# Performance work log

Hardware: AMD Instinct MI355X
Metric: run time of the kernel (lower is better)

The kernel has to match this reference:

```python
import jax, jax.numpy as jnp
import numpy as np

BATCH = 64
N_FEAT = 50000
UNITS = 1024
NNZ = 2_000_000


def setup_inputs() -> dict:
    key = jax.random.key(0)
    k1, k2, k3, k4 = jax.random.split(key, 4)
    x = jax.random.normal(k1, (BATCH, N_FEAT), dtype=jnp.float32)
    # one trainable weight per nonzero of the sparse kernel
    w = jax.random.normal(k2, (NNZ,), dtype=jnp.float32) * 0.02
    row_idx = jax.random.randint(k3, (NNZ,), 0, N_FEAT, dtype=jnp.int32)
    col_idx = jax.random.randint(k4, (NNZ,), 0, UNITS, dtype=jnp.int32)
    return {"x": x, "w": w, "row_idx": row_idx, "col_idx": col_idx}


def reference(x, w, row_idx, col_idx):
    # out[b, u] = sum_{k : col_idx[k]==u} x[b, row_idx[k]] * w[k]
    # == tf.sparse.sparse_dense_matmul(x, SparseTensor(indices, w, [N_FEAT, UNITS]))
    vals = x[:, row_idx] * w  # [batch, nnz] gather + elementwise scale
    out = jnp.zeros((x.shape[0], UNITS), dtype=x.dtype).at[:, col_idx].add(vals)
    return out
```

## Files before the change

### kernel.cpp

```cpp
#include <hip/hip_runtime.h>
#include <hip/hip_bf16.h>

#define BATCH 64
#define UNITS 1024
#define CHUNK 8192
#define JB 32

typedef unsigned int u32;
typedef unsigned short u16;

__global__ __launch_bounds__(256)
void zero4_kernel(uint4* __restrict__ p, int n4) {
    int i = blockIdx.x * 256 + threadIdx.x;
    const int stride = gridDim.x * 256;
    const uint4 z = make_uint4(0u, 0u, 0u, 0u);
    for (; i < n4; i += stride) p[i] = z;
}

__global__ __launch_bounds__(256)
void prep_kernel(const float* __restrict__ x, u16* __restrict__ xT,
                 const int* __restrict__ col, u32* __restrict__ hist2,
                 int nfeat, int nT, int nnz) {
    __shared__ float tile[64][65];
    __shared__ u32 lh[UNITS];
    const int bid = blockIdx.x;
    const int tid = threadIdx.x;
    if (bid < nT) {
        const int c0 = bid * 64;
        const int tx = tid & 63, ty = tid >> 6;
        for (int b = ty; b < 64; b += 4) {
            int c = c0 + tx;
            if (c < nfeat) tile[b][tx] = x[(size_t)b * nfeat + c];
        }
        __syncthreads();
        for (int i = ty; i < 64; i += 4) {
            int c = c0 + i;
            if (c < nfeat) {
                __hip_bfloat16 h = __float2bfloat16(tile[tx][i]);
                xT[(size_t)c * 64 + tx] = *(u16*)&h;
            }
        }
    } else {
        const int g = bid - nT;
        for (int i = tid; i < UNITS; i += 256) lh[i] = 0u;
        __syncthreads();
        const int g0 = g * CHUNK;
        const int n = min(CHUNK, nnz - g0);
        for (int i = tid; i < n; i += 256)
            atomicAdd(&lh[col[g0 + i]], 1u);
        __syncthreads();
        for (int c = tid; c < UNITS; c += 256)
            hist2[(size_t)g * UNITS + c] = lh[c];
    }
}

__global__ __launch_bounds__(1024)
void scanA_kernel(const u32* __restrict__ hist2, u32* __restrict__ partial,
                  int nchunk) {
    const int j = blockIdx.x, c = threadIdx.x;
    const int gs = j * JB, ge = min(gs + JB, nchunk);
    u32 s = 0;
#pragma unroll 8
    for (int g = gs; g < ge; ++g) s += hist2[(size_t)g * UNITS + c];
    partial[(size_t)j * UNITS + c] = s;
}

__global__ __launch_bounds__(1024)
void scanB_kernel(const u32* __restrict__ partial, u32* __restrict__ jb,
                  u32* __restrict__ col_start, int nblk) {
    const int c = threadIdx.x;
    u32 tot = 0;
    for (int j = 0; j < nblk; ++j) tot += partial[(size_t)j * UNITS + c];
    __shared__ u32 a[UNITS];
    a[c] = tot;
    __syncthreads();
    for (int off = 1; off < UNITS; off <<= 1) {
        u32 add = (c >= off) ? a[c - off] : 0u;
        u32 v = a[c];
        __syncthreads();
        a[c] = v + add;
        __syncthreads();
    }
    u32 run = a[c] - tot;
    col_start[c] = run;
    if (c == UNITS - 1) col_start[UNITS] = a[UNITS - 1];
    for (int j = 0; j < nblk; ++j) {
        jb[(size_t)j * UNITS + c] = run;
        run += partial[(size_t)j * UNITS + c];
    }
}

__global__ __launch_bounds__(512)
void reorder_kernel(const int* __restrict__ row, const int* __restrict__ col,
                    const float* __restrict__ w, const u32* __restrict__ hist2,
                    const u32* __restrict__ jb, u32* __restrict__ sorted, int nnz) {
    __shared__ u32 cur[UNITS];
    const int tid = threadIdx.x;
    const int g = blockIdx.x;
    const int j = g / JB, gs = j * JB;
    for (int c = tid; c < UNITS; c += 512) {
        u32 v = jb[(size_t)j * UNITS + c];
#pragma unroll 4
        for (int gp = gs; gp < g; ++gp) v += hist2[(size_t)gp * UNITS + c];
        cur[c] = v;
    }
    __syncthreads();
    const int g0 = g * CHUNK;
    const int n = min(CHUNK, nnz - g0);
#pragma unroll 4
    for (int i = tid; i < n; i += 512) {
        const int k = g0 + i;
        const u32 c = (u32)col[k];
        __hip_bfloat16 h = __float2bfloat16(w[k]);
        const u32 pk = ((u32)(*(const u16*)&h) << 16) | (u32)row[k];
        const u32 lo = atomicAdd(&cur[c], 1u);
        sorted[lo] = pk;
    }
}

__global__ __launch_bounds__(256)
void gather_kernel(const u16* __restrict__ xTu, const u32* __restrict__ sorted,
                   const u32* __restrict__ col_start, float* __restrict__ out) {
    const int u = blockIdx.x;
    const int tid = threadIdx.x;
    const int wv = tid >> 6, lane = tid & 63;
    const u32 s = col_start[u], e = col_start[u + 1];
    float acc0 = 0.f, acc1 = 0.f, acc2 = 0.f, acc3 = 0.f;
    for (u32 b0 = s + (u32)wv * 64u; b0 < e; b0 += 256u) {
        u32 pk = 0u;
        if (b0 + (u32)lane < e) pk = sorted[b0 + (u32)lane];
#pragma unroll
        for (int t = 0; t < 64; t += 4) {
            const u32 e0 = (u32)__builtin_amdgcn_readlane((int)pk, t);
            const u32 e1 = (u32)__builtin_amdgcn_readlane((int)pk, t + 1);
            const u32 e2 = (u32)__builtin_amdgcn_readlane((int)pk, t + 2);
            const u32 e3 = (u32)__builtin_amdgcn_readlane((int)pk, t + 3);
            const float x0 = __uint_as_float(((u32)xTu[(size_t)(e0 & 0xffffu) * 64 + lane]) << 16);
            const float x1 = __uint_as_float(((u32)xTu[(size_t)(e1 & 0xffffu) * 64 + lane]) << 16);
            const float x2 = __uint_as_float(((u32)xTu[(size_t)(e2 & 0xffffu) * 64 + lane]) << 16);
            const float x3 = __uint_as_float(((u32)xTu[(size_t)(e3 & 0xffffu) * 64 + lane]) << 16);
            acc0 = fmaf(x0, __uint_as_float(e0 & 0xffff0000u), acc0);
            acc1 = fmaf(x1, __uint_as_float(e1 & 0xffff0000u), acc1);
            acc2 = fmaf(x2, __uint_as_float(e2 & 0xffff0000u), acc2);
            acc3 = fmaf(x3, __uint_as_float(e3 & 0xffff0000u), acc3);
        }
    }
    float tot = (acc0 + acc1) + (acc2 + acc3);
    __shared__ float red[4][64];
    red[wv][lane] = tot;
    __syncthreads();
    if (wv == 0)
        out[(size_t)lane * UNITS + u] =
            red[0][lane] + red[1][lane] + red[2][lane] + red[3][lane];
}

__global__ __launch_bounds__(1024, 1)
void scatter_fallback_kernel(const u16* __restrict__ xT, const float* __restrict__ w,
                             const int* __restrict__ row_idx, const int* __restrict__ col_idx,
                             float* __restrict__ out, int nnz) {
    extern __shared__ float priv[];
    const int tid = threadIdx.x;
    for (int i = tid; i < 32 * UNITS; i += 1024) priv[i] = 0.0f;
    __syncthreads();
    const int bid = blockIdx.x, half = bid >> 7, wgIdx = bid & 127;
    const int wave = tid >> 6, lane = tid & 63, h = lane >> 5, bl = lane & 31;
    const int per = (nnz + 127) >> 7;
    const int k0 = wgIdx * per, kend = min(k0 + per, nnz);
    const u16* xTh = xT + half * 32 + bl;
    for (int k = k0 + wave * 2 + h; k < kend; k += 32) {
        const int r = row_idx[k], c = col_idx[k];
        const float xv = __uint_as_float(((u32)xTh[(size_t)r * 64]) << 16);
        atomicAdd(&priv[c * 32 + bl], xv * w[k]);
    }
    __syncthreads();
    for (int i = tid; i < 32 * UNITS; i += 1024) {
        int c = i >> 5, b = half * 32 + (i & 31);
        unsafeAtomicAdd(&out[b * UNITS + c], priv[i]);
    }
}

__global__ __launch_bounds__(256)
void fallback_kernel(const float* __restrict__ x, const float* __restrict__ w,
                     const int* __restrict__ row_idx, const int* __restrict__ col_idx,
                     float* __restrict__ out, int nnz, int nfeat) {
    const int nwaves = (gridDim.x * blockDim.x) >> 6;
    const int wid = (blockIdx.x * blockDim.x + threadIdx.x) >> 6;
    const int lane = threadIdx.x & 63;
    for (int k = wid; k < nnz; k += nwaves) {
        const int r = row_idx[k], c = col_idx[k];
        unsafeAtomicAdd(&out[lane * UNITS + c], x[(size_t)lane * nfeat + r] * w[k]);
    }
}

static inline size_t align256(size_t v) { return (v + 255) & ~(size_t)255; }

extern "C" void kernel_launch(void* const* d_in, const int* in_sizes, int n_in,
                              void* d_out, int out_size, void* d_ws, size_t ws_size,
                              hipStream_t stream) {
    const float* x       = (const float*)d_in[0];
    const float* w       = (const float*)d_in[1];
    const int*   row_idx = (const int*)d_in[2];
    const int*   col_idx = (const int*)d_in[3];
    float*       out     = (float*)d_out;
    const int    nnz     = in_sizes[1];
    const int    nfeat   = in_sizes[0] / BATCH;
    const int    nchunk  = (nnz + CHUNK - 1) / CHUNK;
    const int    nblk    = (nchunk + JB - 1) / JB;
    const int    nT      = (nfeat + 63) / 64;

    const size_t xT_bytes = (size_t)nfeat * 64 * sizeof(u16);
    size_t o = align256(xT_bytes);
    const size_t sorted_off = o;  o = align256(o + (size_t)nnz * sizeof(u32));
    const size_t hist2_off  = o;  o = align256(o + (size_t)nchunk * UNITS * sizeof(u32));
    const size_t part_off   = o;  o = align256(o + (size_t)nblk * UNITS * sizeof(u32));
    const size_t jb_off     = o;  o = align256(o + (size_t)nblk * UNITS * sizeof(u32));
    const size_t cs_off     = o;  o = align256(o + (UNITS + 1) * sizeof(u32));

    if (ws_size >= o && nfeat <= 65536 && nblk <= 64) {
        u16* xT        = (u16*)d_ws;
        u32* sorted    = (u32*)((char*)d_ws + sorted_off);
        u32* hist2     = (u32*)((char*)d_ws + hist2_off);
        u32* partial   = (u32*)((char*)d_ws + part_off);
        u32* jb        = (u32*)((char*)d_ws + jb_off);
        u32* col_start = (u32*)((char*)d_ws + cs_off);

        prep_kernel<<<nT + nchunk, 256, 0, stream>>>(x, xT, col_idx, hist2,
                                                     nfeat, nT, nnz);
        scanA_kernel<<<nblk, 1024, 0, stream>>>(hist2, partial, nchunk);
        scanB_kernel<<<1, 1024, 0, stream>>>(partial, jb, col_start, nblk);
        reorder_kernel<<<nchunk, 512, 0, stream>>>(row_idx, col_idx, w, hist2,
                                                   jb, sorted, nnz);
        gather_kernel<<<UNITS, 256, 0, stream>>>(xT, sorted, col_start, out);
    } else if (ws_size >= xT_bytes) {
        u16* xT = (u16*)d_ws;
        const int nOut4 = (out_size * 4 + 15) / 16;
        zero4_kernel<<<64, 256, 0, stream>>>((uint4*)out, nOut4);
        dim3 tb(256);
        prep_kernel<<<nT, 256, 0, stream>>>(x, xT, col_idx, nullptr, nfeat, nT, 0);
        scatter_fallback_kernel<<<256, 1024, 32 * UNITS * sizeof(float), stream>>>(
            xT, w, row_idx, col_idx, out, nnz);
    } else {
        const int nOut4 = (out_size * 4 + 15) / 16;
        zero4_kernel<<<64, 256, 0, stream>>>((uint4*)out, nOut4);
        fallback_kernel<<<2048, 256, 0, stream>>>(x, w, row_idx, col_idx, out, nnz, nfeat);
    }
}
```

Before: 140.1 us.

## Split gather per unit across four blocks with atomic reduction; batch reorder loads

The gather kernel now launches four blocks per output unit. Each block takes an interleaved quarter of that unit's sorted nonzeros, and the results are combined with float atomic adds into an output that is zeroed beforehand. This raises parallelism from 1024 blocks to 4096, which helps fill the GPU. In exchange it adds a zeroing kernel launch and global atomics, and the summation order becomes nondeterministic. Separately, the reorder kernel's full-chunk path batches eight loads before issuing its LDS atomics and stores, to increase memory-level parallelism.

```diff
diff --git a/kernel.cpp b/kernel.cpp
--- a/kernel.cpp
+++ b/kernel.cpp
@@ -5,6 +5,7 @@
 #define UNITS 1024
 #define CHUNK 8192
 #define JB 32
+#define NSPLIT 4
 
 typedef unsigned int u32;
 typedef unsigned short u16;
@@ -107,26 +108,43 @@
     __syncthreads();
     const int g0 = g * CHUNK;
     const int n = min(CHUNK, nnz - g0);
-#pragma unroll 4
-    for (int i = tid; i < n; i += 512) {
-        const int k = g0 + i;
-        const u32 c = (u32)col[k];
-        __hip_bfloat16 h = __float2bfloat16(w[k]);
-        const u32 pk = ((u32)(*(const u16*)&h) << 16) | (u32)row[k];
-        const u32 lo = atomicAdd(&cur[c], 1u);
-        sorted[lo] = pk;
+    if (n == CHUNK) {
+        for (int j2 = 0; j2 < CHUNK / 512; j2 += 8) {
+            u32 cc[8], pk[8], lo[8];
+#pragma unroll
+            for (int q = 0; q < 8; ++q) {
+                const int k = g0 + tid + 512 * (j2 + q);
+                cc[q] = (u32)col[k];
+                __hip_bfloat16 h = __float2bfloat16(w[k]);
+                pk[q] = ((u32)(*(const u16*)&h) << 16) | (u32)row[k];
+            }
+#pragma unroll
+            for (int q = 0; q < 8; ++q) lo[q] = atomicAdd(&cur[cc[q]], 1u);
+#pragma unroll
+            for (int q = 0; q < 8; ++q) sorted[lo[q]] = pk[q];
+        }
+    } else {
+        for (int i = tid; i < n; i += 512) {
+            const int k = g0 + i;
+            const u32 c = (u32)col[k];
+            __hip_bfloat16 h = __float2bfloat16(w[k]);
+            const u32 pk = ((u32)(*(const u16*)&h) << 16) | (u32)row[k];
+            const u32 lo = atomicAdd(&cur[c], 1u);
+            sorted[lo] = pk;
+        }
     }
 }
 
 __global__ __launch_bounds__(256)
 void gather_kernel(const u16* __restrict__ xTu, const u32* __restrict__ sorted,
                    const u32* __restrict__ col_start, float* __restrict__ out) {
-    const int u = blockIdx.x;
+    const int u = blockIdx.x >> 2;
+    const int part = blockIdx.x & 3;
     const int tid = threadIdx.x;
     const int wv = tid >> 6, lane = tid & 63;
     const u32 s = col_start[u], e = col_start[u + 1];
     float acc0 = 0.f, acc1 = 0.f, acc2 = 0.f, acc3 = 0.f;
-    for (u32 b0 = s + (u32)wv * 64u; b0 < e; b0 += 256u) {
+    for (u32 b0 = s + (u32)(part * 4 + wv) * 64u; b0 < e; b0 += (u32)(NSPLIT * 4) * 64u) {
         u32 pk = 0u;
         if (b0 + (u32)lane < e) pk = sorted[b0 + (u32)lane];
 #pragma unroll
@@ -135,10 +153,14 @@
             const u32 e1 = (u32)__builtin_amdgcn_readlane((int)pk, t + 1);
             const u32 e2 = (u32)__builtin_amdgcn_readlane((int)pk, t + 2);
             const u32 e3 = (u32)__builtin_amdgcn_readlane((int)pk, t + 3);
-            const float x0 = __uint_as_float(((u32)xTu[(size_t)(e0 & 0xffffu) * 64 + lane]) << 16);
-            const float x1 = __uint_as_float(((u32)xTu[(size_t)(e1 & 0xffffu) * 64 + lane]) << 16);
-            const float x2 = __uint_as_float(((u32)xTu[(size_t)(e2 & 0xffffu) * 64 + lane]) << 16);
-            const float x3 = __uint_as_float(((u32)xTu[(size_t)(e3 & 0xffffu) * 64 + lane]) << 16);
+            const u16* p0 = xTu + ((e0 & 0xffffu) << 6);
+            const u16* p1 = xTu + ((e1 & 0xffffu) << 6);
+            const u16* p2 = xTu + ((e2 & 0xffffu) << 6);
+            const u16* p3 = xTu + ((e3 & 0xffffu) << 6);
+            const float x0 = __uint_as_float(((u32)p0[lane]) << 16);
+            const float x1 = __uint_as_float(((u32)p1[lane]) << 16);
+            const float x2 = __uint_as_float(((u32)p2[lane]) << 16);
+            const float x3 = __uint_as_float(((u32)p3[lane]) << 16);
             acc0 = fmaf(x0, __uint_as_float(e0 & 0xffff0000u), acc0);
             acc1 = fmaf(x1, __uint_as_float(e1 & 0xffff0000u), acc1);
             acc2 = fmaf(x2, __uint_as_float(e2 & 0xffff0000u), acc2);
@@ -150,8 +172,8 @@
     red[wv][lane] = tot;
     __syncthreads();
     if (wv == 0)
-        out[(size_t)lane * UNITS + u] =
-            red[0][lane] + red[1][lane] + red[2][lane] + red[3][lane];
+        unsafeAtomicAdd(&out[(size_t)lane * UNITS + u],
+                        red[0][lane] + red[1][lane] + red[2][lane] + red[3][lane]);
 }
 
 __global__ __launch_bounds__(1024, 1)
@@ -216,6 +238,8 @@
     const size_t jb_off     = o;  o = align256(o + (size_t)nblk * UNITS * sizeof(u32));
     const size_t cs_off     = o;  o = align256(o + (UNITS + 1) * sizeof(u32));
 
+    const int nOut4 = (out_size * 4 + 15) / 16;
+
     if (ws_size >= o && nfeat <= 65536 && nblk <= 64) {
         u16* xT        = (u16*)d_ws;
         u32* sorted    = (u32*)((char*)d_ws + sorted_off);
@@ -224,23 +248,21 @@
         u32* jb        = (u32*)((char*)d_ws + jb_off);
         u32* col_start = (u32*)((char*)d_ws + cs_off);
 
+        zero4_kernel<<<64, 256, 0, stream>>>((uint4*)out, nOut4);
         prep_kernel<<<nT + nchunk, 256, 0, stream>>>(x, xT, col_idx, hist2,
                                                      nfeat, nT, nnz);
         scanA_kernel<<<nblk, 1024, 0, stream>>>(hist2, partial, nchunk);
         scanB_kernel<<<1, 1024, 0, stream>>>(partial, jb, col_start, nblk);
         reorder_kernel<<<nchunk, 512, 0, stream>>>(row_idx, col_idx, w, hist2,
                                                    jb, sorted, nnz);
-        gather_kernel<<<UNITS, 256, 0, stream>>>(xT, sorted, col_start, out);
+        gather_kernel<<<UNITS * NSPLIT, 256, 0, stream>>>(xT, sorted, col_start, out);
     } else if (ws_size >= xT_bytes) {
         u16* xT = (u16*)d_ws;
-        const int nOut4 = (out_size * 4 + 15) / 16;
         zero4_kernel<<<64, 256, 0, stream>>>((uint4*)out, nOut4);
-        dim3 tb(256);
         prep_kernel<<<nT, 256, 0, stream>>>(x, xT, col_idx, nullptr, nfeat, nT, 0);
         scatter_fallback_kernel<<<256, 1024, 32 * UNITS * sizeof(float), stream>>>(
             xT, w, row_idx, col_idx, out, nnz);
     } else {
-        const int nOut4 = (out_size * 4 + 15) / 16;
         zero4_kernel<<<64, 256, 0, stream>>>((uint4*)out, nOut4);
         fallback_kernel<<<2048, 256, 0, stream>>>(x, w, row_idx, col_idx, out, nnz, nfeat);
     }
```

Measured after the change: 146.2 us. +4.3%, slower.

## Fuse histogram scans into reorder kernel and double chunk size

Applied to the files above, without the earlier changes.

Removes the two separate scan kernels. Each reorder block now reads the whole per-chunk histogram, computes the global column totals and its own chunk prefix, and runs a double-buffered shared-memory scan itself. CHUNK doubles to 16384, which cuts the number of chunks to about 123, and the reorder loop is batched 8-wide so loads overlap LDS atomics. This saves two kernel launches and their serial dependency. In exchange every block redundantly reads the full histogram (nchunk×1024 words) and does a 1024-wide scan, and the larger chunks give fewer blocks for the prep histogram and reorder phases.

```diff
diff --git a/kernel.cpp b/kernel.cpp
--- a/kernel.cpp
+++ b/kernel.cpp
@@ -3,8 +3,7 @@
 
 #define BATCH 64
 #define UNITS 1024
-#define CHUNK 8192
-#define JB 32
+#define CHUNK 16384
 
 typedef unsigned int u32;
 typedef unsigned short u16;
@@ -55,66 +54,72 @@
 }
 
 __global__ __launch_bounds__(1024)
-void scanA_kernel(const u32* __restrict__ hist2, u32* __restrict__ partial,
-                  int nchunk) {
-    const int j = blockIdx.x, c = threadIdx.x;
-    const int gs = j * JB, ge = min(gs + JB, nchunk);
-    u32 s = 0;
-#pragma unroll 8
-    for (int g = gs; g < ge; ++g) s += hist2[(size_t)g * UNITS + c];
-    partial[(size_t)j * UNITS + c] = s;
-}
-
-__global__ __launch_bounds__(1024)
-void scanB_kernel(const u32* __restrict__ partial, u32* __restrict__ jb,
-                  u32* __restrict__ col_start, int nblk) {
+void reorder_scan_kernel(const int* __restrict__ row, const int* __restrict__ col,
+                         const float* __restrict__ w, const u32* __restrict__ hist2,
+                         u32* __restrict__ col_start, u32* __restrict__ sorted,
+                         int nchunk, int nnz) {
+    __shared__ u32 aA[UNITS], aB[UNITS], cur[UNITS];
     const int c = threadIdx.x;
-    u32 tot = 0;
-    for (int j = 0; j < nblk; ++j) tot += partial[(size_t)j * UNITS + c];
-    __shared__ u32 a[UNITS];
-    a[c] = tot;
-    __syncthreads();
+    const int g = blockIdx.x;
+    u32 tot = 0, pre = 0;
+    int gp = 0;
+    for (; gp + 4 <= nchunk; gp += 4) {
+        const u32 h0 = hist2[(size_t)(gp + 0) * UNITS + c];
+        const u32 h1 = hist2[(size_t)(gp + 1) * UNITS + c];
+        const u32 h2 = hist2[(size_t)(gp + 2) * UNITS + c];
+        const u32 h3 = hist2[(size_t)(gp + 3) * UNITS + c];
+        tot += (h0 + h1) + (h2 + h3);
+        pre += (gp + 0 < g ? h0 : 0u) + (gp + 1 < g ? h1 : 0u) +
+               (gp + 2 < g ? h2 : 0u) + (gp + 3 < g ? h3 : 0u);
+    }
+    for (; gp < nchunk; ++gp) {
+        const u32 h = hist2[(size_t)gp * UNITS + c];
+        tot += h;
+        if (gp < g) pre += h;
+    }
+    aA[c] = tot;
+    __syncthreads();
+    u32* src = aA;
+    u32* dst = aB;
     for (int off = 1; off < UNITS; off <<= 1) {
-        u32 add = (c >= off) ? a[c - off] : 0u;
-        u32 v = a[c];
-        __syncthreads();
-        a[c] = v + add;
-        __syncthreads();
-    }
-    u32 run = a[c] - tot;
-    col_start[c] = run;
-    if (c == UNITS - 1) col_start[UNITS] = a[UNITS - 1];
-    for (int j = 0; j < nblk; ++j) {
-        jb[(size_t)j * UNITS + c] = run;
-        run += partial[(size_t)j * UNITS + c];
-    }
-}
-
-__global__ __launch_bounds__(512)
-void reorder_kernel(const int* __restrict__ row, const int* __restrict__ col,
-                    const float* __restrict__ w, const u32* __restrict__ hist2,
-                    const u32* __restrict__ jb, u32* __restrict__ sorted, int nnz) {
-    __shared__ u32 cur[UNITS];
-    const int tid = threadIdx.x;
-    const int g = blockIdx.x;
-    const int j = g / JB, gs = j * JB;
-    for (int c = tid; c < UNITS; c += 512) {
-        u32 v = jb[(size_t)j * UNITS + c];
-#pragma unroll 4
-        for (int gp = gs; gp < g; ++gp) v += hist2[(size_t)gp * UNITS + c];
-        cur[c] = v;
+        dst[c] = src[c] + ((c >= off) ? src[c - off] : 0u);
+        __syncthreads();
+        u32* t = src; src = dst; dst = t;
+    }
+    const u32 incl = src[c];
+    const u32 excl = incl - tot;
+    cur[c] = excl + pre;
+    if (g == 0) {
+        col_start[c] = excl;
+        if (c == UNITS - 1) col_start[UNITS] = incl;
     }
     __syncthreads();
     const int g0 = g * CHUNK;
     const int n = min(CHUNK, nnz - g0);
-#pragma unroll 4
-    for (int i = tid; i < n; i += 512) {
-        const int k = g0 + i;
-        const u32 c = (u32)col[k];
-        __hip_bfloat16 h = __float2bfloat16(w[k]);
-        const u32 pk = ((u32)(*(const u16*)&h) << 16) | (u32)row[k];
-        const u32 lo = atomicAdd(&cur[c], 1u);
-        sorted[lo] = pk;
+    if (n == CHUNK) {
+        for (int j2 = 0; j2 < CHUNK / 1024; j2 += 8) {
+            u32 cc[8], pk[8], lo[8];
+#pragma unroll
+            for (int q = 0; q < 8; ++q) {
+                const int k = g0 + c + 1024 * (j2 + q);
+                cc[q] = (u32)col[k];
+                __hip_bfloat16 h = __float2bfloat16(w[k]);
+                pk[q] = ((u32)(*(const u16*)&h) << 16) | (u32)row[k];
+            }
+#pragma unroll
+            for (int q = 0; q < 8; ++q) lo[q] = atomicAdd(&cur[cc[q]], 1u);
+#pragma unroll
+            for (int q = 0; q < 8; ++q) sorted[lo[q]] = pk[q];
+        }
+    } else {
+        for (int i = c; i < n; i += 1024) {
+            const int k = g0 + i;
+            const u32 cc = (u32)col[k];
+            __hip_bfloat16 h = __float2bfloat16(w[k]);
+            const u32 pk = ((u32)(*(const u16*)&h) << 16) | (u32)row[k];
+            const u32 lo = atomicAdd(&cur[cc], 1u);
+            sorted[lo] = pk;
+        }
     }
 }
 
@@ -205,42 +210,34 @@
     const int    nnz     = in_sizes[1];
     const int    nfeat   = in_sizes[0] / BATCH;
     const int    nchunk  = (nnz + CHUNK - 1) / CHUNK;
-    const int    nblk    = (nchunk + JB - 1) / JB;
     const int    nT      = (nfeat + 63) / 64;
 
     const size_t xT_bytes = (size_t)nfeat * 64 * sizeof(u16);
     size_t o = align256(xT_bytes);
     const size_t sorted_off = o;  o = align256(o + (size_t)nnz * sizeof(u32));
     const size_t hist2_off  = o;  o = align256(o + (size_t)nchunk * UNITS * sizeof(u32));
-    const size_t part_off   = o;  o = align256(o + (size_t)nblk * UNITS * sizeof(u32));
-    const size_t jb_off     = o;  o = align256(o + (size_t)nblk * UNITS * sizeof(u32));
     const size_t cs_off     = o;  o = align256(o + (UNITS + 1) * sizeof(u32));
 
-    if (ws_size >= o && nfeat <= 65536 && nblk <= 64) {
+    const int nOut4 = (out_size * 4 + 15) / 16;
+
+    if (ws_size >= o && nfeat <= 65536 && nchunk <= 2048) {
         u16* xT        = (u16*)d_ws;
         u32* sorted    = (u32*)((char*)d_ws + sorted_off);
         u32* hist2     = (u32*)((char*)d_ws + hist2_off);
-        u32* partial   = (u32*)((char*)d_ws + part_off);
-        u32* jb        = (u32*)((char*)d_ws + jb_off);
         u32* col_start = (u32*)((char*)d_ws + cs_off);
 
         prep_kernel<<<nT + nchunk, 256, 0, stream>>>(x, xT, col_idx, hist2,
                                                      nfeat, nT, nnz);
-        scanA_kernel<<<nblk, 1024, 0, stream>>>(hist2, partial, nchunk);
-        scanB_kernel<<<1, 1024, 0, stream>>>(partial, jb, col_start, nblk);
-        reorder_kernel<<<nchunk, 512, 0, stream>>>(row_idx, col_idx, w, hist2,
-                                                   jb, sorted, nnz);
+        reorder_scan_kernel<<<nchunk, 1024, 0, stream>>>(
+            row_idx, col_idx, w, hist2, col_start, sorted, nchunk, nnz);
         gather_kernel<<<UNITS, 256, 0, stream>>>(xT, sorted, col_start, out);
     } else if (ws_size >= xT_bytes) {
         u16* xT = (u16*)d_ws;
-        const int nOut4 = (out_size * 4 + 15) / 16;
         zero4_kernel<<<64, 256, 0, stream>>>((uint4*)out, nOut4);
-        dim3 tb(256);
         prep_kernel<<<nT, 256, 0, stream>>>(x, xT, col_idx, nullptr, nfeat, nT, 0);
         scatter_fallback_kernel<<<256, 1024, 32 * UNITS * sizeof(float), stream>>>(
             xT, w, row_idx, col_idx, out, nnz);
     } else {
-        const int nOut4 = (out_size * 4 + 15) / 16;
         zero4_kernel<<<64, 256, 0, stream>>>((uint4*)out, nOut4);
         fallback_kernel<<<2048, 256, 0, stream>>>(x, w, row_idx, col_idx, out, nnz, nfeat);
     }
```

Measured after the change: 147.7 us. +5.5%, slower.
